# Kernel tuning notes

Measured on AMD Instinct MI355X. Metric: run time of the kernel, lower is better.

## Reference

```python
import jax, jax.numpy as jnp
import numpy as np

EMBED_DIM = 1024
NUM_HEADS = 16
HEAD_DIM = EMBED_DIM // NUM_HEADS
LAMBDA_ENTANGLE = 0.35


def setup_inputs() -> dict:
    key = jax.random.key(0)
    ks = jax.random.split(key, 10)
    B, S, D = 2, 2048, EMBED_DIM
    init = 1.0 / np.sqrt(D)  # mimic nn.Linear uniform init scale
    x = jax.random.normal(ks[0], (B, S, D), dtype=jnp.float32)
    Wq = jax.random.uniform(ks[1], (D, D), jnp.float32, -init, init)
    bq = jax.random.uniform(ks[2], (D,), jnp.float32, -init, init)
    Wk = jax.random.uniform(ks[3], (D, D), jnp.float32, -init, init)
    bk = jax.random.uniform(ks[4], (D,), jnp.float32, -init, init)
    Wv = jax.random.uniform(ks[5], (D, D), jnp.float32, -init, init)
    bv = jax.random.uniform(ks[6], (D,), jnp.float32, -init, init)
    Wo = jax.random.uniform(ks[7], (D, D), jnp.float32, -init, init)
    bo = jax.random.uniform(ks[8], (D,), jnp.float32, -init, init)
    J_attn = jax.random.normal(ks[9], (NUM_HEADS, HEAD_DIM, HEAD_DIM), dtype=jnp.float32) * 0.02
    lambda_attn = jnp.asarray(LAMBDA_ENTANGLE, dtype=jnp.float32)
    return {"x": x, "Wq": Wq, "bq": bq, "Wk": Wk, "bk": bk, "Wv": Wv, "bv": bv,
            "Wo": Wo, "bo": bo, "J_attn": J_attn, "lambda_attn": lambda_attn}


def reference(x, Wq, bq, Wk, bk, Wv, bv, Wo, bo, J_attn, lambda_attn):
    B, S, D = x.shape
    H, Hd = NUM_HEADS, HEAD_DIM
    scale = jnp.sqrt(jnp.asarray(Hd, dtype=x.dtype))

    def heads(W, b):
        # (B,S,D) @ (D,D) + b -> (B,H,S,Hd)
        y = jnp.einsum('bsd,ed->bse', x, W) + b
        return y.reshape(B, S, H, Hd).transpose(0, 2, 1, 3)

    Q = heads(Wq, bq)
    K = heads(Wk, bk)
    V = heads(Wv, bv)

    scores = jnp.einsum('bhid,bhjd->bhij', Q, K) / scale
    # bilinear entanglement correction: tanh(Q) J tanh(K)^T
    QJ = jnp.einsum('bhid,hde->bhie', jnp.tanh(Q), J_attn)  # (B,H,S,Hd)
    delta = jnp.einsum('bhie,bhje->bhij', QJ, jnp.tanh(K))
    scores = scores + lambda_attn * delta

    causal = jnp.triu(jnp.ones((S, S), dtype=bool), k=1)
    scores = jnp.where(causal, -jnp.inf, scores)

    probs = jax.nn.softmax(scores, axis=-1)
    out = jnp.einsum('bhij,bhjd->bhid', probs, V)  # (B,H,S,Hd)
    out = out.transpose(0, 2, 1, 3).reshape(B, S, D)
    return jnp.einsum('bsd,ed->bse', out, Wo) + bo
```

## Files before the change

kernel.cpp:

```cpp
#include <hip/hip_runtime.h>
#include <hip/hip_bf16.h>

typedef unsigned short u16;
typedef __bf16 bf16x8 __attribute__((ext_vector_type(8)));
typedef float f32x4 __attribute__((ext_vector_type(4)));
typedef unsigned short u16x4 __attribute__((ext_vector_type(4)));

#define MFMA16(a, b, c) __builtin_amdgcn_mfma_f32_16x16x32_bf16(a, b, c, 0, 0, 0)

#define EMB 1024
#define SEQ 2048
#define NH 16
#define HD 64
#define LOG2E 1.4426950408889634f

#define GLOAD_LDS16(g, l) __builtin_amdgcn_global_load_lds( \
    (const __attribute__((address_space(1))) unsigned int*)(g), \
    (__attribute__((address_space(3))) unsigned int*)(l), 16, 0, 0)

__device__ __forceinline__ float b2f(u16 u) {
    union { unsigned int i; float f; } v; v.i = ((unsigned int)u) << 16; return v.f;
}
__device__ __forceinline__ u16 f2b(float f) {
    __hip_bfloat16 h = __float2bfloat16(f);
    return *reinterpret_cast<u16*>(&h);
}
__device__ __forceinline__ u16x4 pack4(float a, float b, float c, float d) {
    union { __hip_bfloat162 h2[2]; u16x4 u; } r;
    r.h2[0] = __float22bfloat162_rn(float2{a, b});
    r.h2[1] = __float22bfloat162_rn(float2{c, d});
    return r.u;
}
__device__ __forceinline__ bf16x8 ldfrag(const u16* p) {
    return *reinterpret_cast<const bf16x8*>(p);
}
__device__ __forceinline__ bf16x8 cvt8(const float* p) {
    const float4 a = *reinterpret_cast<const float4*>(p);
    const float4 b = *reinterpret_cast<const float4*>(p + 4);
    union { u16x4 q[2]; bf16x8 v; } r;
    r.q[0] = pack4(a.x, a.y, a.z, a.w);
    r.q[1] = pack4(b.x, b.y, b.z, b.w);
    return r.v;
}
__device__ __forceinline__ float fast_tanh(float x) {
    float t = exp2f(x * (2.0f * LOG2E));
    return 1.0f - 2.0f * __builtin_amdgcn_rcpf(t + 1.0f);
}
__device__ __forceinline__ bf16x8 tanh8(bf16x8 v) {
    union { bf16x8 v; u16 u[8]; } in; in.v = v;
    float o[8];
#pragma unroll
    for (int e = 0; e < 8; e++) o[e] = fast_tanh(b2f(in.u[e]));
    union { u16x4 q[2]; bf16x8 v; } r;
    r.q[0] = pack4(o[0], o[1], o[2], o[3]);
    r.q[1] = pack4(o[4], o[5], o[6], o[7]);
    return r.v;
}

__global__ __launch_bounds__(256) void cvt_all(
        const float* __restrict__ x,  const float* __restrict__ Wq,
        const float* __restrict__ Wk, const float* __restrict__ Wv,
        const float* __restrict__ Wo, u16* __restrict__ dst)
{
    size_t i = ((size_t)blockIdx.x * 256 + threadIdx.x) * 8;
    const float* src; size_t off;
    if (i < 4194304) { src = x; off = i; }
    else {
        size_t j = i - 4194304; int w = (int)(j >> 20); off = j & 1048575;
        src = (w == 0) ? Wq : (w == 1) ? Wk : (w == 2) ? Wv : Wo;
    }
    *(bf16x8*)&dst[i] = cvt8(src + off);
}

template<int MI>
__global__ __launch_bounds__(256) void gemm_epi(
        const u16* __restrict__ A,
        const u16* __restrict__ W0, const float* __restrict__ B0,
        const u16* __restrict__ W1, const float* __restrict__ B1,
        const u16* __restrict__ W2, const float* __restrict__ B2,
        const float* __restrict__ lam,
        u16* __restrict__ Qa, u16* __restrict__ Ka, u16* __restrict__ Vt,
        float* __restrict__ out, int modeBase)
{
    const int mode = modeBase + blockIdx.z;
    const u16* W; const float* bias;
    if (blockIdx.z == 0)      { W = W0; bias = B0; }
    else if (blockIdx.z == 1) { W = W1; bias = B1; }
    else                      { W = W2; bias = B2; }

    __shared__ __attribute__((aligned(16))) u16 sA[MI * 32 * 32];
    __shared__ __attribute__((aligned(16))) u16 sB[128 * 32];

    const int t = threadIdx.x;
    const int w = t >> 6, L = t & 63;
    const int wm = w >> 1, wn = w & 1;
    const int lr = L & 15, lq = L >> 4;
    const int wbase = t & 192;
    const int m0 = blockIdx.y * (MI * 32), n0 = blockIdx.x * 128;

    f32x4 acc[MI][4];
#pragma unroll
    for (int i = 0; i < MI; i++)
#pragma unroll
        for (int j = 0; j < 4; j++) { f32x4 z = {0.f, 0.f, 0.f, 0.f}; acc[i][j] = z; }

    for (int k0 = 0; k0 < EMB; k0 += 32) {
        __syncthreads();
#pragma unroll
        for (int q = 0; q < MI / 2; q++) {
            int c = q * 256 + t;
            int row = c >> 2, cc = c & 3;
            int col8 = cc ^ (row & 3);
            GLOAD_LDS16(&A[(size_t)(m0 + row) * EMB + k0 + col8 * 8],
                        &sA[(q * 256 + wbase) * 8]);
        }
#pragma unroll
        for (int q = 0; q < 2; q++) {
            int c = q * 256 + t;
            int row = c >> 2, cc = c & 3;
            int col8 = cc ^ (row & 3);
            GLOAD_LDS16(&W[(size_t)(n0 + row) * EMB + k0 + col8 * 8],
                        &sB[(q * 256 + wbase) * 8]);
        }
        __syncthreads();
        bf16x8 af[MI], bfr[4];
#pragma unroll
        for (int mi = 0; mi < MI; mi++) {
            int row = wm * (MI * 16) + mi * 16 + lr;
            af[mi] = ldfrag(&sA[(row * 4 + (lq ^ (row & 3))) * 8]);
        }
#pragma unroll
        for (int ni = 0; ni < 4; ni++) {
            int row = wn * 64 + ni * 16 + lr;
            bfr[ni] = ldfrag(&sB[(row * 4 + (lq ^ (row & 3))) * 8]);
        }
#pragma unroll
        for (int mi = 0; mi < MI; mi++)
#pragma unroll
            for (int ni = 0; ni < 4; ni++)
                acc[mi][ni] = MFMA16(af[mi], bfr[ni], acc[mi][ni]);
    }

    const float lamf = lam[0];
#pragma unroll
    for (int mi = 0; mi < MI; mi++)
#pragma unroll
        for (int ni = 0; ni < 4; ni++) {
            int mb = m0 + wm * (MI * 16) + mi * 16 + lq * 4;
            int n  = n0 + wn * 64 + ni * 16 + lr;
            float bv = bias[n];
            if (mode == 3) {
#pragma unroll
                for (int r = 0; r < 4; r++)
                    out[(size_t)(mb + r) * EMB + n] = acc[mi][ni][r] + bv;
            } else {
                int b = mb >> 11, s0 = mb & 2047;
                int h = n >> 6,  d = n & 63;
                if (mode == 0) {
#pragma unroll
                    for (int r = 0; r < 4; r++) {
                        float val = acc[mi][ni][r] + bv;
                        size_t i128 = ((size_t)(b * NH + h) * SEQ + s0 + r) * 128 + d;
                        Qa[i128]      = f2b(val * (0.125f * LOG2E));
                        Qa[i128 + 64] = f2b(lamf * LOG2E * fast_tanh(val));
                    }
                } else if (mode == 1) {
#pragma unroll
                    for (int r = 0; r < 4; r++) {
                        float val = acc[mi][ni][r] + bv;
                        Ka[((size_t)(b * NH + h) * SEQ + s0 + r) * 128 + d] = f2b(val);
                    }
                } else {
                    u16x4 pk = pack4(acc[mi][ni][0] + bv, acc[mi][ni][1] + bv,
                                     acc[mi][ni][2] + bv, acc[mi][ni][3] + bv);
                    *(u16x4*)&Vt[((size_t)(b * NH + h) * HD + d) * SEQ + s0] = pk;
                }
            }
        }
}

__global__ __launch_bounds__(256) void ukern(
        const float* __restrict__ J, u16* __restrict__ Ka)
{
    __shared__ __attribute__((aligned(16))) u16 sJ[64 * 72];
    const int t = threadIdx.x, w = t >> 6, L = t & 63, lr = L & 15, lq = L >> 4;
    const int rt = blockIdx.x, bh = blockIdx.y, h = bh & 15;

#pragma unroll
    for (int i = 0; i < 2; i++) {
        int c = t + 256 * i;
        int row = c >> 3, col = (c & 7) * 8;
        *(bf16x8*)&sJ[row * 72 + col] = cvt8(&J[(size_t)h * 4096 + row * 64 + col]);
    }
    __syncthreads();

    const u16* krow = &Ka[((size_t)bh * SEQ + rt * 64 + w * 16 + lr) * 128];
    bf16x8 a0 = tanh8(ldfrag(krow + lq * 8));
    bf16x8 a1 = tanh8(ldfrag(krow + lq * 8 + 32));
#pragma unroll
    for (int nt = 0; nt < 4; nt++) {
        f32x4 acc = {0.f, 0.f, 0.f, 0.f};
        acc = MFMA16(a0, ldfrag(&sJ[(nt * 16 + lr) * 72 + lq * 8]), acc);
        acc = MFMA16(a1, ldfrag(&sJ[(nt * 16 + lr) * 72 + lq * 8 + 32]), acc);
#pragma unroll
        for (int r = 0; r < 4; r++) {
            int j = rt * 64 + w * 16 + lq * 4 + r;
            Ka[((size_t)bh * SEQ + j) * 128 + 64 + nt * 16 + lr] = f2b(acc[r]);
        }
    }
}

__global__ __launch_bounds__(256) void flash(
        const u16* __restrict__ Qa, const u16* __restrict__ Ka,
        const u16* __restrict__ Vt, u16* __restrict__ attn)
{
    __shared__ __attribute__((aligned(16))) u16 sK[64 * 128];
    __shared__ __attribute__((aligned(16))) u16 sVt[64 * 64];
    __shared__ __attribute__((aligned(16))) u16 sP[64 * 72];

    const int t = threadIdx.x, w = t >> 6, L = t & 63, lr = L & 15, lq = L >> 4;
    const int c = blockIdx.x, s_ = blockIdx.y;
    const int bh = c & 31, p = c >> 5;
    const int qt = (s_ == 0) ? p : (s_ == 1) ? 15 - p : (s_ == 2) ? 16 + p : 31 - p;
    const int qm = qt * 64;
    const int i_l = w * 16 + lr;
    const int wbase = t & 192;

    bf16x8 qf[4];
    {
        const u16* qrow = Qa + ((size_t)bh * SEQ + qm + i_l) * 128;
#pragma unroll
        for (int s = 0; s < 4; s++) qf[s] = ldfrag(qrow + s * 32 + lq * 8);
    }

    f32x4 Ot[4];
#pragma unroll
    for (int i = 0; i < 4; i++) { f32x4 z = {0.f, 0.f, 0.f, 0.f}; Ot[i] = z; }
    float lsum = 0.f;

    for (int kt = 0; kt <= qt; kt++) {
        const int kn = kt * 64;
        __syncthreads();
#pragma unroll
        for (int q = 0; q < 4; q++) {
            int cch = q * 256 + t;
            int row = cch >> 4, cc = cch & 15;
            int col8 = cc ^ (row & 15);
            GLOAD_LDS16(&Ka[((size_t)bh * SEQ + kn + row) * 128 + col8 * 8],
                        &sK[(q * 256 + wbase) * 8]);
        }
#pragma unroll
        for (int q = 0; q < 2; q++) {
            int cch = q * 256 + t;
            int d = cch >> 3, cc = cch & 7;
            int j8 = cc ^ (d & 7);
            GLOAD_LDS16(&Vt[((size_t)bh * HD + d) * SEQ + kn + j8 * 8],
                        &sVt[(q * 256 + wbase) * 8]);
        }
        __syncthreads();

        f32x4 sc[4];
#pragma unroll
        for (int mt = 0; mt < 4; mt++) {
            int j = mt * 16 + lr;
            f32x4 a = {0.f, 0.f, 0.f, 0.f};
#pragma unroll
            for (int s = 0; s < 4; s++) {
                int q = s * 4 + lq;
                a = MFMA16(ldfrag(&sK[(j * 16 + (q ^ (j & 15))) * 8]), qf[s], a);
            }
            sc[mt] = a;
        }
        if (kt == qt) {
#pragma unroll
            for (int mt = 0; mt < 4; mt++)
#pragma unroll
                for (int r = 0; r < 4; r++)
                    if (mt * 16 + lq * 4 + r > i_l) sc[mt][r] = -INFINITY;
        }
#pragma unroll
        for (int mt = 0; mt < 4; mt++)
#pragma unroll
            for (int r = 0; r < 4; r++) {
                float e = exp2f(sc[mt][r]);
                sc[mt][r] = e;
                lsum += e;
            }
#pragma unroll
        for (int mt = 0; mt < 4; mt++)
            *(u16x4*)&sP[i_l * 72 + mt * 16 + lq * 4] =
                pack4(sc[mt][0], sc[mt][1], sc[mt][2], sc[mt][3]);
#pragma unroll
        for (int s2 = 0; s2 < 2; s2++) {
            bf16x8 pf = ldfrag(&sP[i_l * 72 + s2 * 32 + lq * 8]);
#pragma unroll
            for (int mt = 0; mt < 4; mt++) {
                int d = mt * 16 + lr;
                int q = s2 * 4 + lq;
                Ot[mt] = MFMA16(ldfrag(&sVt[(d * 8 + (q ^ (d & 7))) * 8]), pf, Ot[mt]);
            }
        }
    }

    lsum += __shfl_xor(lsum, 16);
    lsum += __shfl_xor(lsum, 32);
    const float inv = __builtin_amdgcn_rcpf(lsum) *
                      (2.0f - lsum * __builtin_amdgcn_rcpf(lsum));
    const int b = bh >> 4, h = bh & 15;
    const size_t base = ((size_t)(b * SEQ + qm + i_l)) * EMB + h * HD;
#pragma unroll
    for (int mt = 0; mt < 4; mt++)
        *(u16x4*)&attn[base + mt * 16 + lq * 4] =
            pack4(Ot[mt][0] * inv, Ot[mt][1] * inv, Ot[mt][2] * inv, Ot[mt][3] * inv);
}

extern "C" void kernel_launch(void* const* d_in, const int* in_sizes, int n_in,
                              void* d_out, int out_size, void* d_ws, size_t ws_size,
                              hipStream_t stream)
{
    const float* x   = (const float*)d_in[0];
    const float* Wq  = (const float*)d_in[1];
    const float* bq  = (const float*)d_in[2];
    const float* Wk  = (const float*)d_in[3];
    const float* bk  = (const float*)d_in[4];
    const float* Wv  = (const float*)d_in[5];
    const float* bv  = (const float*)d_in[6];
    const float* Wo  = (const float*)d_in[7];
    const float* bo  = (const float*)d_in[8];
    const float* J   = (const float*)d_in[9];
    const float* lam = (const float*)d_in[10];

    u16* ws  = (u16*)d_ws;
    u16* xb  = ws;
    u16* Wqb = xb  + (size_t)4096 * 1024;
    u16* Wkb = Wqb + (size_t)1024 * 1024;
    u16* Wvb = Wkb + (size_t)1024 * 1024;
    u16* Wob = Wvb + (size_t)1024 * 1024;
    u16* Qa  = Wob + (size_t)1024 * 1024;
    u16* Ka  = Qa  + (size_t)32 * 2048 * 128;
    u16* Vt  = Ka  + (size_t)32 * 2048 * 128;
    u16* attn = xb;
    float* dout = (float*)d_out;

    dim3 blk(256);
    cvt_all<<<dim3(4096), blk, 0, stream>>>(x, Wq, Wk, Wv, Wo, ws);
    gemm_epi<4><<<dim3(8, 32, 3), blk, 0, stream>>>(
        xb, Wqb, bq, Wkb, bk, Wvb, bv, lam, Qa, Ka, Vt, dout, 0);
    ukern<<<dim3(32, 32), blk, 0, stream>>>(J, Ka);
    flash<<<dim3(256, 4), blk, 0, stream>>>(Qa, Ka, Vt, attn);
    gemm_epi<2><<<dim3(8, 64, 1), blk, 0, stream>>>(
        attn, Wob, bo, Wob, bo, Wob, bo, lam, Qa, Ka, Vt, dout, 3);
}
```

Baseline: 215.0 us.

## Process two query tiles per flash block and deepen GEMM K-tile to 64

The flash kernel now handles 128 query rows per block as two 64-row groups sharing each loaded K/V tile, halving K/V global loads and LDS fragment reads per query. Causal masking is adjusted per group, with one extra fully masked tile computed for the first group. The projection GEMM doubles its K step to 64 with wider swizzle and adds an occupancy hint, halving barrier count per K. Risks are fewer flash blocks (less parallelism), higher register pressure, and more LDS use.

```diff
diff --git a/kernel.cpp b/kernel.cpp
--- a/kernel.cpp
+++ b/kernel.cpp
@@ -73,7 +73,7 @@
 }
 
 template<int MI>
-__global__ __launch_bounds__(256) void gemm_epi(
+__global__ __launch_bounds__(256, 4) void gemm_epi(
         const u16* __restrict__ A,
         const u16* __restrict__ W0, const float* __restrict__ B0,
         const u16* __restrict__ W1, const float* __restrict__ B1,
@@ -88,8 +88,8 @@
     else if (blockIdx.z == 1) { W = W1; bias = B1; }
     else                      { W = W2; bias = B2; }
 
-    __shared__ __attribute__((aligned(16))) u16 sA[MI * 32 * 32];
-    __shared__ __attribute__((aligned(16))) u16 sB[128 * 32];
+    __shared__ __attribute__((aligned(16))) u16 sA[MI * 32 * 64];
+    __shared__ __attribute__((aligned(16))) u16 sB[128 * 64];
 
     const int t = threadIdx.x;
     const int w = t >> 6, L = t & 63;
@@ -104,41 +104,44 @@
 #pragma unroll
         for (int j = 0; j < 4; j++) { f32x4 z = {0.f, 0.f, 0.f, 0.f}; acc[i][j] = z; }
 
-    for (int k0 = 0; k0 < EMB; k0 += 32) {
+    for (int k0 = 0; k0 < EMB; k0 += 64) {
         __syncthreads();
 #pragma unroll
-        for (int q = 0; q < MI / 2; q++) {
+        for (int q = 0; q < MI; q++) {
             int c = q * 256 + t;
-            int row = c >> 2, cc = c & 3;
-            int col8 = cc ^ (row & 3);
+            int row = c >> 3, cc = c & 7;
+            int col8 = cc ^ (row & 7);
             GLOAD_LDS16(&A[(size_t)(m0 + row) * EMB + k0 + col8 * 8],
                         &sA[(q * 256 + wbase) * 8]);
         }
 #pragma unroll
-        for (int q = 0; q < 2; q++) {
+        for (int q = 0; q < 4; q++) {
             int c = q * 256 + t;
-            int row = c >> 2, cc = c & 3;
-            int col8 = cc ^ (row & 3);
+            int row = c >> 3, cc = c & 7;
+            int col8 = cc ^ (row & 7);
             GLOAD_LDS16(&W[(size_t)(n0 + row) * EMB + k0 + col8 * 8],
                         &sB[(q * 256 + wbase) * 8]);
         }
         __syncthreads();
-        bf16x8 af[MI], bfr[4];
-#pragma unroll
-        for (int mi = 0; mi < MI; mi++) {
-            int row = wm * (MI * 16) + mi * 16 + lr;
-            af[mi] = ldfrag(&sA[(row * 4 + (lq ^ (row & 3))) * 8]);
-        }
-#pragma unroll
-        for (int ni = 0; ni < 4; ni++) {
-            int row = wn * 64 + ni * 16 + lr;
-            bfr[ni] = ldfrag(&sB[(row * 4 + (lq ^ (row & 3))) * 8]);
-        }
-#pragma unroll
-        for (int mi = 0; mi < MI; mi++)
-#pragma unroll
-            for (int ni = 0; ni < 4; ni++)
-                acc[mi][ni] = MFMA16(af[mi], bfr[ni], acc[mi][ni]);
+#pragma unroll
+        for (int s = 0; s < 2; s++) {
+            bf16x8 af[MI], bfr[4];
+#pragma unroll
+            for (int mi = 0; mi < MI; mi++) {
+                int row = wm * (MI * 16) + mi * 16 + lr;
+                af[mi] = ldfrag(&sA[(row * 8 + ((s * 4 + lq) ^ (row & 7))) * 8]);
+            }
+#pragma unroll
+            for (int ni = 0; ni < 4; ni++) {
+                int row = wn * 64 + ni * 16 + lr;
+                bfr[ni] = ldfrag(&sB[(row * 8 + ((s * 4 + lq) ^ (row & 7))) * 8]);
+            }
+#pragma unroll
+            for (int mi = 0; mi < MI; mi++)
+#pragma unroll
+                for (int ni = 0; ni < 4; ni++)
+                    acc[mi][ni] = MFMA16(af[mi], bfr[ni], acc[mi][ni]);
+        }
     }
 
     const float lamf = lam[0];
@@ -216,29 +219,34 @@
 {
     __shared__ __attribute__((aligned(16))) u16 sK[64 * 128];
     __shared__ __attribute__((aligned(16))) u16 sVt[64 * 64];
-    __shared__ __attribute__((aligned(16))) u16 sP[64 * 72];
+    __shared__ __attribute__((aligned(16))) u16 sP[128 * 72];
 
     const int t = threadIdx.x, w = t >> 6, L = t & 63, lr = L & 15, lq = L >> 4;
-    const int c = blockIdx.x, s_ = blockIdx.y;
-    const int bh = c & 31, p = c >> 5;
-    const int qt = (s_ == 0) ? p : (s_ == 1) ? 15 - p : (s_ == 2) ? 16 + p : 31 - p;
-    const int qm = qt * 64;
+    const int bh = blockIdx.x & 31, p = blockIdx.x >> 5;
+    const int qt = blockIdx.y ? 15 - p : p;
+    const int qm = qt * 128;
     const int i_l = w * 16 + lr;
     const int wbase = t & 192;
-
-    bf16x8 qf[4];
-    {
-        const u16* qrow = Qa + ((size_t)bh * SEQ + qm + i_l) * 128;
-#pragma unroll
-        for (int s = 0; s < 4; s++) qf[s] = ldfrag(qrow + s * 32 + lq * 8);
-    }
-
-    f32x4 Ot[4];
-#pragma unroll
-    for (int i = 0; i < 4; i++) { f32x4 z = {0.f, 0.f, 0.f, 0.f}; Ot[i] = z; }
-    float lsum = 0.f;
-
-    for (int kt = 0; kt <= qt; kt++) {
+    const u16* Kbase = Ka + (size_t)bh * SEQ * 128;
+    const u16* Vbase = Vt + (size_t)bh * HD * SEQ;
+
+    bf16x8 qf[2][4];
+#pragma unroll
+    for (int g = 0; g < 2; g++) {
+        const u16* qrow = Qa + ((size_t)bh * SEQ + qm + g * 64 + i_l) * 128;
+#pragma unroll
+        for (int s = 0; s < 4; s++) qf[g][s] = ldfrag(qrow + s * 32 + lq * 8);
+    }
+
+    f32x4 Ot[2][4];
+#pragma unroll
+    for (int g = 0; g < 2; g++)
+#pragma unroll
+        for (int i = 0; i < 4; i++) { f32x4 z = {0.f, 0.f, 0.f, 0.f}; Ot[g][i] = z; }
+    float lsum[2] = {0.f, 0.f};
+
+    const int ktmax = 2 * qt + 1;
+    for (int kt = 0; kt <= ktmax; kt++) {
         const int kn = kt * 64;
         __syncthreads();
 #pragma unroll
@@ -246,7 +254,7 @@
             int cch = q * 256 + t;
             int row = cch >> 4, cc = cch & 15;
             int col8 = cc ^ (row & 15);
-            GLOAD_LDS16(&Ka[((size_t)bh * SEQ + kn + row) * 128 + col8 * 8],
+            GLOAD_LDS16(&Kbase[(size_t)(kn + row) * 128 + col8 * 8],
                         &sK[(q * 256 + wbase) * 8]);
         }
 #pragma unroll
@@ -254,64 +262,82 @@
             int cch = q * 256 + t;
             int d = cch >> 3, cc = cch & 7;
             int j8 = cc ^ (d & 7);
-            GLOAD_LDS16(&Vt[((size_t)bh * HD + d) * SEQ + kn + j8 * 8],
+            GLOAD_LDS16(&Vbase[(size_t)d * SEQ + kn + j8 * 8],
                         &sVt[(q * 256 + wbase) * 8]);
         }
         __syncthreads();
 
-        f32x4 sc[4];
+        f32x4 sc[2][4];
+#pragma unroll
+        for (int g = 0; g < 2; g++)
+#pragma unroll
+            for (int mt = 0; mt < 4; mt++) { f32x4 z = {0.f,0.f,0.f,0.f}; sc[g][mt] = z; }
 #pragma unroll
         for (int mt = 0; mt < 4; mt++) {
             int j = mt * 16 + lr;
-            f32x4 a = {0.f, 0.f, 0.f, 0.f};
 #pragma unroll
             for (int s = 0; s < 4; s++) {
-                int q = s * 4 + lq;
-                a = MFMA16(ldfrag(&sK[(j * 16 + (q ^ (j & 15))) * 8]), qf[s], a);
-            }
-            sc[mt] = a;
-        }
-        if (kt == qt) {
+                bf16x8 kf = ldfrag(&sK[(j * 16 + ((s * 4 + lq) ^ (j & 15))) * 8]);
+                sc[0][mt] = MFMA16(kf, qf[0][s], sc[0][mt]);
+                sc[1][mt] = MFMA16(kf, qf[1][s], sc[1][mt]);
+            }
+        }
+        if (kt >= ktmax - 1) {
+            const int thr0 = (kt == ktmax) ? -1  : i_l;
+            const int thr1 = (kt == ktmax) ? i_l : 63;
 #pragma unroll
             for (int mt = 0; mt < 4; mt++)
 #pragma unroll
-                for (int r = 0; r < 4; r++)
-                    if (mt * 16 + lq * 4 + r > i_l) sc[mt][r] = -INFINITY;
-        }
-#pragma unroll
-        for (int mt = 0; mt < 4; mt++)
-#pragma unroll
-            for (int r = 0; r < 4; r++) {
-                float e = exp2f(sc[mt][r]);
-                sc[mt][r] = e;
-                lsum += e;
-            }
-#pragma unroll
-        for (int mt = 0; mt < 4; mt++)
-            *(u16x4*)&sP[i_l * 72 + mt * 16 + lq * 4] =
-                pack4(sc[mt][0], sc[mt][1], sc[mt][2], sc[mt][3]);
+                for (int r = 0; r < 4; r++) {
+                    int j = mt * 16 + lq * 4 + r;
+                    if (j > thr0) sc[0][mt][r] = -INFINITY;
+                    if (j > thr1) sc[1][mt][r] = -INFINITY;
+                }
+        }
+#pragma unroll
+        for (int g = 0; g < 2; g++) {
+#pragma unroll
+            for (int mt = 0; mt < 4; mt++)
+#pragma unroll
+                for (int r = 0; r < 4; r++) {
+                    float e = exp2f(sc[g][mt][r]);
+                    sc[g][mt][r] = e;
+                    lsum[g] += e;
+                }
+#pragma unroll
+            for (int mt = 0; mt < 4; mt++)
+                *(u16x4*)&sP[(g * 64 + i_l) * 72 + mt * 16 + lq * 4] =
+                    pack4(sc[g][mt][0], sc[g][mt][1], sc[g][mt][2], sc[g][mt][3]);
+        }
 #pragma unroll
         for (int s2 = 0; s2 < 2; s2++) {
-            bf16x8 pf = ldfrag(&sP[i_l * 72 + s2 * 32 + lq * 8]);
+            bf16x8 pf0 = ldfrag(&sP[(i_l) * 72 + s2 * 32 + lq * 8]);
+            bf16x8 pf1 = ldfrag(&sP[(64 + i_l) * 72 + s2 * 32 + lq * 8]);
 #pragma unroll
             for (int mt = 0; mt < 4; mt++) {
                 int d = mt * 16 + lr;
-                int q = s2 * 4 + lq;
-                Ot[mt] = MFMA16(ldfrag(&sVt[(d * 8 + (q ^ (d & 7))) * 8]), pf, Ot[mt]);
-            }
-        }
-    }
-
-    lsum += __shfl_xor(lsum, 16);
-    lsum += __shfl_xor(lsum, 32);
-    const float inv = __builtin_amdgcn_rcpf(lsum) *
-                      (2.0f - lsum * __builtin_amdgcn_rcpf(lsum));
+                bf16x8 vf = ldfrag(&sVt[(d * 8 + ((s2 * 4 + lq) ^ (d & 7))) * 8]);
+                Ot[0][mt] = MFMA16(vf, pf0, Ot[0][mt]);
+                Ot[1][mt] = MFMA16(vf, pf1, Ot[1][mt]);
+            }
+        }
+    }
+
     const int b = bh >> 4, h = bh & 15;
-    const size_t base = ((size_t)(b * SEQ + qm + i_l)) * EMB + h * HD;
-#pragma unroll
-    for (int mt = 0; mt < 4; mt++)
-        *(u16x4*)&attn[base + mt * 16 + lq * 4] =
-            pack4(Ot[mt][0] * inv, Ot[mt][1] * inv, Ot[mt][2] * inv, Ot[mt][3] * inv);
+#pragma unroll
+    for (int g = 0; g < 2; g++) {
+        float ls = lsum[g];
+        ls += __shfl_xor(ls, 16);
+        ls += __shfl_xor(ls, 32);
+        const float r0 = __builtin_amdgcn_rcpf(ls);
+        const float inv = r0 * (2.0f - ls * r0);
+        const size_t base = ((size_t)(b * SEQ + qm + g * 64 + i_l)) * EMB + h * HD;
+#pragma unroll
+        for (int mt = 0; mt < 4; mt++)
+            *(u16x4*)&attn[base + mt * 16 + lq * 4] =
+                pack4(Ot[g][mt][0] * inv, Ot[g][mt][1] * inv,
+                      Ot[g][mt][2] * inv, Ot[g][mt][3] * inv);
+    }
 }
 
 extern "C" void kernel_launch(void* const* d_in, const int* in_sizes, int n_in,
@@ -347,7 +373,7 @@
     gemm_epi<4><<<dim3(8, 32, 3), blk, 0, stream>>>(
         xb, Wqb, bq, Wkb, bk, Wvb, bv, lam, Qa, Ka, Vt, dout, 0);
     ukern<<<dim3(32, 32), blk, 0, stream>>>(J, Ka);
-    flash<<<dim3(256, 4), blk, 0, stream>>>(Qa, Ka, Vt, attn);
+    flash<<<dim3(256, 2), blk, 0, stream>>>(Qa, Ka, Vt, attn);
     gemm_epi<2><<<dim3(8, 64, 1), blk, 0, stream>>>(
         attn, Wob, bo, Wob, bo, Wob, bo, lam, Qa, Ka, Vt, dout, 3);
 }
```

New measurement: 210.8 us. 1.02x faster.
